# Kernel tuning notes

Hardware: AMD Instinct MI355X
Metric: run time of the kernel (lower is better)

Reference implementation:

```python
import jax, jax.numpy as jnp
import numpy as np

B, T, L = 32, 128, 16
VOCAB, E, H = 256, 256, 512


def setup_inputs() -> dict:
    key = jax.random.key(0)
    ks = jax.random.split(key, 7)
    char_seq_padded = jax.random.randint(ks[0], (B, T, L), 0, VOCAB, dtype=jnp.int32)
    char_lengths = jax.random.randint(ks[1], (B, T), 1, L + 1, dtype=jnp.int32)
    emb = jax.random.normal(ks[2], (VOCAB, E), dtype=jnp.float32) * 0.1
    emb = emb.at[0].set(0.0)  # padding_idx=0 -> zero row
    s_ih = 1.0 / np.sqrt(H)
    W_ih = jax.random.uniform(ks[3], (4 * H, E), jnp.float32, -s_ih, s_ih)
    W_hh = jax.random.uniform(ks[4], (4 * H, H), jnp.float32, -s_ih, s_ih)
    b_ih = jax.random.uniform(ks[5], (4 * H,), jnp.float32, -s_ih, s_ih)
    b_hh = jax.random.uniform(ks[6], (4 * H,), jnp.float32, -s_ih, s_ih)
    return {"char_seq_padded": char_seq_padded, "char_lengths": char_lengths,
            "emb": emb, "W_ih": W_ih, "W_hh": W_hh, "b_ih": b_ih, "b_hh": b_hh}


def _char_lstm(char_seq_padded, char_lengths, emb, W_ih, W_hh, b_ih, b_hh):
    b, t, l = char_seq_padded.shape
    h_dim = W_hh.shape[1]
    idx = char_seq_padded.reshape(b * t, l).T          # [L, B*T]
    lens = char_lengths.reshape(b * t)                  # [B*T]
    bias = b_ih + b_hh

    def step(carry, inp):
        h, c = carry
        ids, tt = inp
        x = emb[ids]                                    # [BT, E]
        gates = x @ W_ih.T + h @ W_hh.T + bias          # [BT, 4H]
        i, f, g, o = jnp.split(gates, 4, axis=-1)       # torch order i,f,g,o
        i = jax.nn.sigmoid(i)
        f = jax.nn.sigmoid(f)
        g = jnp.tanh(g)
        o = jax.nn.sigmoid(o)
        c_new = f * c + i * g
        h_new = o * jnp.tanh(c_new)
        m = (lens > tt).astype(h.dtype)[:, None]        # length mask blend
        h = h_new * m + h * (1.0 - m)
        c = c_new * m + c * (1.0 - m)
        return (h, c), None

    h0 = jnp.zeros((b * t, h_dim), dtype=emb.dtype)
    c0 = jnp.zeros((b * t, h_dim), dtype=emb.dtype)
    (h, _), _ = jax.lax.scan(step, (h0, c0), (idx, jnp.arange(l)))
    return h.reshape(b, t, h_dim)


def reference(char_seq_padded, char_lengths, emb, W_ih, W_hh, b_ih, b_hh):
    return _char_lstm(char_seq_padded, char_lengths, emb, W_ih, W_hh, b_ih, b_hh)
```

## Files before the change

### kernel.cpp

```cpp
#include <hip/hip_runtime.h>
#include <hip/hip_bf16.h>

typedef __attribute__((ext_vector_type(8))) short short8;
typedef __attribute__((ext_vector_type(4))) short short4v;
typedef __attribute__((ext_vector_type(4))) float floatx4;

#define EDIM 256
#define HDIM 512
#define LDIM 16
#define NCOL 2048
#define BM 256
#define KC 32

__device__ __forceinline__ float fsigmoid(float x){ return 1.0f/(1.0f+__expf(-x)); }
__device__ __forceinline__ float ftanh(float x){ return 2.0f/(1.0f+__expf(-2.0f*x))-1.0f; }
__device__ __forceinline__ float bf2f(short s){
    union { unsigned u; float f; } cv; cv.u = ((unsigned)(unsigned short)s) << 16; return cv.f;
}
__device__ __forceinline__ unsigned short f2bf_bits(float v){
    union { __hip_bfloat16 h; unsigned short u; } cv;
    cv.h = __float2bfloat16(v); return cv.u;
}

__device__ __forceinline__ short8 aload16(const short* p) {
    union { unsigned long long q[2]; short8 s; } u;
    u.q[0] = __hip_atomic_load((const unsigned long long*)p,
                               __ATOMIC_RELAXED, __HIP_MEMORY_SCOPE_AGENT);
    u.q[1] = __hip_atomic_load((const unsigned long long*)p + 1,
                               __ATOMIC_RELAXED, __HIP_MEMORY_SCOPE_AGENT);
    return u.s;
}
__device__ __forceinline__ void astore_bf16(short* p, float v) {
    __hip_atomic_store((unsigned short*)p, f2bf_bits(v),
                       __ATOMIC_RELAXED, __HIP_MEMORY_SCOPE_AGENT);
}
__device__ __forceinline__ void lds_barrier() {
    asm volatile("s_waitcnt lgkmcnt(0)" ::: "memory");
    __builtin_amdgcn_s_barrier();
}

__device__ __forceinline__ bool detect_bf16(const short* p) {
    bool bf = true;
    for (int i = 0; i < 64; i += 2) {
        int e = (((unsigned short)p[i]) >> 7) & 0xFF;
        if (e > 0x7B) bf = false;
    }
    return bf;
}

__global__ void conv_whh(const void* __restrict__ whhp, short* __restrict__ whh_o,
                         unsigned* __restrict__ bar) {
    if (blockIdx.x == 0)
        for (int i = threadIdx.x; i < 512; i += 256) bar[i] = 0u;
    bool bf = detect_bf16((const short*)whhp);
    int tid = blockIdx.x * blockDim.x + threadIdx.x;
    int stride = gridDim.x * blockDim.x;
    if (bf) {
        const short* s = (const short*)whhp;
        for (int i = tid; i < NCOL * HDIM; i += stride) whh_o[i] = s[i];
    } else {
        const float* s = (const float*)whhp;
        for (int i = tid; i < NCOL * HDIM; i += stride)
            ((__hip_bfloat16*)whh_o)[i] = __float2bfloat16(s[i]);
    }
}

__global__ void build_xg(const void* __restrict__ embp, const void* __restrict__ wihp,
                         const void* __restrict__ bihp, const void* __restrict__ bhhp,
                         short* __restrict__ xg)
{
    __shared__ float es[16][EDIM];
    __shared__ float wsm[32][EDIM + 1];
    bool bf = detect_bf16((const short*)wihp);
    const int idt = blockIdx.x, ct = blockIdx.y, tt = threadIdx.x;

    if (bf) {
        const __hip_bfloat16* e = (const __hip_bfloat16*)embp;
        const __hip_bfloat16* wv = (const __hip_bfloat16*)wihp;
        for (int p = 0; p < 16; ++p) es[p][tt] = __bfloat162float(e[(idt*16+p)*EDIM + tt]);
        for (int p = 0; p < 32; ++p) wsm[p][tt] = __bfloat162float(wv[(ct*32+p)*EDIM + tt]);
    } else {
        const float* e = (const float*)embp;
        const float* wv = (const float*)wihp;
        for (int p = 0; p < 16; ++p) es[p][tt] = e[(idt*16+p)*EDIM + tt];
        for (int p = 0; p < 32; ++p) wsm[p][tt] = wv[(ct*32+p)*EDIM + tt];
    }
    __syncthreads();

    const int col_l = tt & 31, grp = tt >> 5;
    const int col = ct * 32 + col_l;
    float bsum = bf ? (__bfloat162float(((const __hip_bfloat16*)bihp)[col]) +
                       __bfloat162float(((const __hip_bfloat16*)bhhp)[col]))
                    : (((const float*)bihp)[col] + ((const float*)bhhp)[col]);
    float a0 = 0.f, a1 = 0.f;
    for (int k = 0; k < EDIM; ++k) {
        float wv = wsm[col_l][k];
        a0 += es[grp*2+0][k] * wv;
        a1 += es[grp*2+1][k] * wv;
    }
    const int jj = col & (HDIM - 1), gsel = col >> 9;
    ((__hip_bfloat16*)xg)[(idt*16 + grp*2 + 0)*NCOL + jj*4 + gsel] = __float2bfloat16(a0 + bsum);
    ((__hip_bfloat16*)xg)[(idt*16 + grp*2 + 1)*NCOL + jj*4 + gsel] = __float2bfloat16(a1 + bsum);
}

__launch_bounds__(512, 2)
__global__ void lstm_fused(const int* __restrict__ seq, const int* __restrict__ lens,
                           const short* __restrict__ whh,
                           const short* __restrict__ xg,
                           short* __restrict__ hb0, short* __restrict__ hb1,
                           float* __restrict__ out,
                           unsigned* __restrict__ bar)
{
    __shared__ __align__(16) short Bs[128 * 512];
    __shared__ __align__(16) short As[2][BM * KC];

    const int f  = blockIdx.x;
    const int mt = ((f & 7) << 1) | ((f >> 3) & 1);
    const int jt = f >> 4;
    const int tid = threadIdx.x;
    const int wave = tid >> 6, lane = tid & 63;
    const int q = lane >> 4, ln = lane & 15;
    const int ms = wave & 3, ns = wave >> 2;
    const int jloc = ns * 16 + ln;
    const int jglob = jt * 32 + jloc;

#pragma unroll
    for (int it = 0; it < 16; ++it) {
        int task = it * 512 + tid;
        int row = task >> 6, seg = task & 63;
        int grow = (row >> 5) * HDIM + jt * 32 + (row & 31);
        short8 v = *(const short8*)(whh + grow * HDIM + seg * 8);
        *(short8*)&Bs[row * 512 + ((seg * 8) ^ ((row & 7) << 3))] = v;
    }

    const int chainbase = mt * BM + ms * 64 + q * 4;
    const int obase = chainbase * HDIM + jglob;
    unsigned* __restrict__ barp = bar + (mt << 5);

    const int srow = tid >> 2, sseg = tid & 3;
    const int g0 = srow * HDIM + sseg * 8;
    const int g1 = (128 + srow) * HDIM + sseg * 8;
    const int l0 = srow * KC + ((sseg * 8) ^ ((srow & 3) << 3));
    const int l1 = (128 + srow) * KC + ((sseg * 8) ^ ((srow & 3) << 3));

    unsigned lnspk[4] = {0u, 0u, 0u, 0u};
#pragma unroll
    for (int e = 0; e < 16; ++e)
        lnspk[e >> 2] |= ((unsigned)lens[chainbase + (e >> 2) * 16 + (e & 3)] & 0xFFu)
                         << ((e & 3) * 8);

    float c_st[16], h_st[16];
#pragma unroll
    for (int e = 0; e < 16; ++e) { c_st[e] = 0.f; h_st[e] = 0.f; }

    int idsN[16];
    short4v xv[16];
#pragma unroll
    for (int e = 0; e < 16; ++e)
        idsN[e] = seq[(chainbase + (e >> 2) * 16 + (e & 3)) * LDIM + 0];
#pragma unroll
    for (int e = 0; e < 16; ++e)
        xv[e] = *(const short4v*)(xg + idsN[e] * NCOL + jglob * 4);

    for (int t = 0; t < LDIM; ++t) {
        const short* hr = (t & 1) ? hb1 : hb0;
        short* hw       = (t & 1) ? hb0 : hb1;
        const bool notlast = (t < LDIM - 1);

        if (notlast) {
#pragma unroll
            for (int e = 0; e < 16; ++e)
                idsN[e] = seq[(chainbase + (e >> 2) * 16 + (e & 3)) * LDIM + t + 1];
        }

        floatx4 acc[4][4];
#pragma unroll
        for (int g = 0; g < 4; ++g)
#pragma unroll
            for (int mf = 0; mf < 4; ++mf) acc[g][mf] = (floatx4){0.f, 0.f, 0.f, 0.f};

        if (t > 0) {
            const short* abase = hr + (size_t)mt * BM * HDIM;
            short8 rq[2][2];
            {
                short8 v0 = aload16(abase + g0);
                short8 v1 = aload16(abase + g1);
                rq[1][0]  = aload16(abase + g0 + KC);
                rq[1][1]  = aload16(abase + g1 + KC);
                *(short8*)&As[0][l0] = v0;
                *(short8*)&As[0][l1] = v1;
            }
            lds_barrier();
#pragma unroll
            for (int kc = 0; kc < 16; ++kc) {
                const int b = kc & 1;
                if (kc < 15) {
                    *(short8*)&As[b ^ 1][l0] = rq[(kc + 1) & 1][0];
                    *(short8*)&As[b ^ 1][l1] = rq[(kc + 1) & 1][1];
                }
                if (kc < 14) {
                    rq[kc & 1][0] = aload16(abase + g0 + (kc + 2) * KC);
                    rq[kc & 1][1] = aload16(abase + g1 + (kc + 2) * KC);
                }
                short8 af[4], bfr[4];
#pragma unroll
                for (int mf = 0; mf < 4; ++mf)
                    af[mf] = *(const short8*)&As[b][(ms * 64 + mf * 16 + ln) * KC +
                                                    ((q * 8) ^ ((ln & 3) << 3))];
#pragma unroll
                for (int g = 0; g < 4; ++g)
                    bfr[g] = *(const short8*)&Bs[(g * 32 + jloc) * 512 +
                                                 ((kc * 32 + q * 8) ^ ((ln & 7) << 3))];
                __builtin_amdgcn_s_setprio(1);
#pragma unroll
                for (int g = 0; g < 4; ++g)
#pragma unroll
                    for (int mf = 0; mf < 4; ++mf)
                        acc[g][mf] = __builtin_amdgcn_mfma_f32_16x16x32_bf16(
                            af[mf], bfr[g], acc[g][mf], 0, 0, 0);
                __builtin_amdgcn_s_setprio(0);
                lds_barrier();
            }
        }

#pragma unroll
        for (int e = 0; e < 16; ++e) {
            const int mf = e >> 2, r = e & 3;
            float p0 = acc[0][mf][r] + bf2f(xv[e][0]);
            float p1 = acc[1][mf][r] + bf2f(xv[e][1]);
            float p2 = acc[2][mf][r] + bf2f(xv[e][2]);
            float p3 = acc[3][mf][r] + bf2f(xv[e][3]);
            float ig = fsigmoid(p0);
            float fg = fsigmoid(p1);
            float gg = ftanh(p2);
            float og = fsigmoid(p3);
            float cn = fg * c_st[e] + ig * gg;
            float hn = og * ftanh(cn);
            bool mk = (int)((lnspk[e >> 2] >> ((e & 3) * 8)) & 0xFFu) > t;
            float hsv = mk ? hn : h_st[e];
            float csv = mk ? cn : c_st[e];
            h_st[e] = hsv; c_st[e] = csv;
            int off = obase + (mf * 16 + r) * HDIM;
            if (notlast) astore_bf16(hw + off, hsv);
            else         out[off] = hsv;
        }

        if (notlast) {
            __syncthreads();
#pragma unroll
            for (int e = 0; e < 16; ++e)
                xv[e] = *(const short4v*)(xg + idsN[e] * NCOL + jglob * 4);
            if (tid == 0) {
                __hip_atomic_fetch_add(barp, 1u, __ATOMIC_RELAXED,
                                       __HIP_MEMORY_SCOPE_AGENT);
                const unsigned target = 16u * (unsigned)(t + 1);
                while (__hip_atomic_load(barp, __ATOMIC_RELAXED,
                                         __HIP_MEMORY_SCOPE_AGENT) < target)
                    __builtin_amdgcn_s_sleep(2);
            }
            __syncthreads();
        }
    }
}

extern "C" void kernel_launch(void* const* d_in, const int* in_sizes, int n_in,
                              void* d_out, int out_size, void* d_ws, size_t ws_size,
                              hipStream_t stream) {
    const int* seq  = (const int*)d_in[0];
    const int* lens = (const int*)d_in[1];

    char* w = (char*)d_ws;
    short* h_even = (short*)w;
    short* h_odd  = (short*)(w + 4u*1024*1024);
    short* xg     = (short*)(w + 8u*1024*1024);
    short* whh_bf = (short*)(w + 9u*1024*1024);
    unsigned* bar = (unsigned*)(w + 11u*1024*1024);
    float* outp   = (float*)d_out;

    conv_whh<<<512, 256, 0, stream>>>(d_in[4], whh_bf, bar);
    build_xg<<<dim3(16, 64), 256, 0, stream>>>(d_in[2], d_in[3], d_in[5], d_in[6], xg);
    lstm_fused<<<256, 512, 0, stream>>>(seq, lens, whh_bf, xg, h_even, h_odd, outp, bar);
}
```

Before: 433.0 us.

## Replace per-step group barrier with fine-grained per-block ready flags

Swaps the per-timestep counter barrier across the 16 column-tile blocks of a row group for per-block step flags. Each consumer waits only on the producer flags covering the K-chunks it is about to load, so staged waits can overlap with MFMA work. A separate consumed flag stops a producer from overwriting a double-buffered h slice before readers have finished with it. This cuts synchronization stalls but adds more atomic polling and depends on delicate ordering with relaxed atomics.

```diff
diff --git a/kernel.cpp b/kernel.cpp
--- a/kernel.cpp
+++ b/kernel.cpp
@@ -34,6 +34,20 @@
     __hip_atomic_store((unsigned short*)p, f2bf_bits(v),
                        __ATOMIC_RELAXED, __HIP_MEMORY_SCOPE_AGENT);
 }
+__device__ __forceinline__ unsigned ald(const unsigned* p) {
+    return __hip_atomic_load(p, __ATOMIC_RELAXED, __HIP_MEMORY_SCOPE_AGENT);
+}
+__device__ __forceinline__ void ast(unsigned* p, unsigned v) {
+    __hip_atomic_store(p, v, __ATOMIC_RELAXED, __HIP_MEMORY_SCOPE_AGENT);
+}
+__device__ __forceinline__ void waitflags4(const unsigned* f, unsigned v) {
+    for (;;) {
+        unsigned a = ald(f + 0), b = ald(f + 1);
+        unsigned c = ald(f + 2), d = ald(f + 3);
+        if (a >= v && b >= v && c >= v && d >= v) break;
+        __builtin_amdgcn_s_sleep(1);
+    }
+}
 __device__ __forceinline__ void lds_barrier() {
     asm volatile("s_waitcnt lgkmcnt(0)" ::: "memory");
     __builtin_amdgcn_s_barrier();
@@ -49,9 +63,9 @@
 }
 
 __global__ void conv_whh(const void* __restrict__ whhp, short* __restrict__ whh_o,
-                         unsigned* __restrict__ bar) {
+                         unsigned* __restrict__ sync) {
     if (blockIdx.x == 0)
-        for (int i = threadIdx.x; i < 512; i += 256) bar[i] = 0u;
+        for (int i = threadIdx.x; i < 9216; i += 256) sync[i] = 0u;
     bool bf = detect_bf16((const short*)whhp);
     int tid = blockIdx.x * blockDim.x + threadIdx.x;
     int stride = gridDim.x * blockDim.x;
@@ -109,7 +123,7 @@
                            const short* __restrict__ xg,
                            short* __restrict__ hb0, short* __restrict__ hb1,
                            float* __restrict__ out,
-                           unsigned* __restrict__ bar)
+                           unsigned* __restrict__ sync)
 {
     __shared__ __align__(16) short Bs[128 * 512];
     __shared__ __align__(16) short As[2][BM * KC];
@@ -124,6 +138,9 @@
     const int jloc = ns * 16 + ln;
     const int jglob = jt * 32 + jloc;
 
+    unsigned* const wd = sync + mt * 16;
+    unsigned* const kd = sync + 1024 + (mt * 16) * 32;
+
 #pragma unroll
     for (int it = 0; it < 16; ++it) {
         int task = it * 512 + tid;
@@ -135,7 +152,6 @@
 
     const int chainbase = mt * BM + ms * 64 + q * 4;
     const int obase = chainbase * HDIM + jglob;
-    unsigned* __restrict__ barp = bar + (mt << 5);
 
     const int srow = tid >> 2, sseg = tid & 3;
     const int g0 = srow * HDIM + sseg * 8;
@@ -180,7 +196,9 @@
             for (int mf = 0; mf < 4; ++mf) acc[g][mf] = (floatx4){0.f, 0.f, 0.f, 0.f};
 
         if (t > 0) {
+            const unsigned si = (unsigned)t;
             const short* abase = hr + (size_t)mt * BM * HDIM;
+            waitflags4(wd + 0, si);
             short8 rq[2][2];
             {
                 short8 v0 = aload16(abase + g0);
@@ -198,6 +216,9 @@
                     *(short8*)&As[b ^ 1][l0] = rq[(kc + 1) & 1][0];
                     *(short8*)&As[b ^ 1][l1] = rq[(kc + 1) & 1][1];
                 }
+                if (kc == 0) waitflags4(wd + 4,  si);
+                if (kc == 4) waitflags4(wd + 8,  si);
+                if (kc == 8) waitflags4(wd + 12, si);
                 if (kc < 14) {
                     rq[kc & 1][0] = aload16(abase + g0 + (kc + 2) * KC);
                     rq[kc & 1][1] = aload16(abase + g1 + (kc + 2) * KC);
@@ -221,6 +242,16 @@
                 __builtin_amdgcn_s_setprio(0);
                 lds_barrier();
             }
+            if (tid == 0) ast(kd + jt * 32, si);
+        }
+
+        if (t >= 2 && t < 15) {
+            if (tid < 16) {
+                const unsigned need = (unsigned)(t - 1);
+                while (ald(kd + tid * 32) < need)
+                    __builtin_amdgcn_s_sleep(1);
+            }
+            __syncthreads();
         }
 
 #pragma unroll
@@ -247,18 +278,10 @@
 
         if (notlast) {
             __syncthreads();
+            if (tid == 0) ast(wd + jt, (unsigned)(t + 1));
 #pragma unroll
             for (int e = 0; e < 16; ++e)
                 xv[e] = *(const short4v*)(xg + idsN[e] * NCOL + jglob * 4);
-            if (tid == 0) {
-                __hip_atomic_fetch_add(barp, 1u, __ATOMIC_RELAXED,
-                                       __HIP_MEMORY_SCOPE_AGENT);
-                const unsigned target = 16u * (unsigned)(t + 1);
-                while (__hip_atomic_load(barp, __ATOMIC_RELAXED,
-                                         __HIP_MEMORY_SCOPE_AGENT) < target)
-                    __builtin_amdgcn_s_sleep(2);
-            }
-            __syncthreads();
         }
     }
 }
@@ -274,10 +297,10 @@
     short* h_odd  = (short*)(w + 4u*1024*1024);
     short* xg     = (short*)(w + 8u*1024*1024);
     short* whh_bf = (short*)(w + 9u*1024*1024);
-    unsigned* bar = (unsigned*)(w + 11u*1024*1024);
+    unsigned* syn = (unsigned*)(w + 11u*1024*1024);
     float* outp   = (float*)d_out;
 
-    conv_whh<<<512, 256, 0, stream>>>(d_in[4], whh_bf, bar);
+    conv_whh<<<512, 256, 0, stream>>>(d_in[4], whh_bf, syn);
     build_xg<<<dim3(16, 64), 256, 0, stream>>>(d_in[2], d_in[3], d_in[5], d_in[6], xg);
-    lstm_fused<<<256, 512, 0, stream>>>(seq, lens, whh_bf, xg, h_even, h_odd, outp, bar);
-}
+    lstm_fused<<<256, 512, 0, stream>>>(seq, lens, whh_bf, xg, h_even, h_odd, outp, syn);
+}
```

New measurement: 463.4 us. +7.0%, slower.

## Split LSTM recurrence into 512 narrower blocks with wave-private A tiles

Applied to the files above, without the earlier changes.

Halves the hidden columns handled per block (16 instead of 32), which doubles the grid to 512 blocks and cuts LDS per block so two blocks can sit on each CU. Each wave now stages only its own 32 rows of the h tile into a single LDS buffer, so the per-k-chunk workgroup barriers are removed. The grid barrier target is doubled to match the larger block count. The x-gate loads are no longer prefetched across the barrier and are issued inside the gate epilogue instead. In exchange, every block rereads the full h tile, so global/L2 traffic for h doubles, and the x-gate load latency becomes exposed.

```diff
diff --git a/kernel.cpp b/kernel.cpp
--- a/kernel.cpp
+++ b/kernel.cpp
@@ -9,7 +9,6 @@
 #define HDIM 512
 #define LDIM 16
 #define NCOL 2048
-#define BM 256
 #define KC 32
 
 __device__ __forceinline__ float fsigmoid(float x){ return 1.0f/(1.0f+__expf(-x)); }
@@ -33,10 +32,6 @@
 __device__ __forceinline__ void astore_bf16(short* p, float v) {
     __hip_atomic_store((unsigned short*)p, f2bf_bits(v),
                        __ATOMIC_RELAXED, __HIP_MEMORY_SCOPE_AGENT);
-}
-__device__ __forceinline__ void lds_barrier() {
-    asm volatile("s_waitcnt lgkmcnt(0)" ::: "memory");
-    __builtin_amdgcn_s_barrier();
 }
 
 __device__ __forceinline__ bool detect_bf16(const short* p) {
@@ -103,7 +98,7 @@
     ((__hip_bfloat16*)xg)[(idt*16 + grp*2 + 1)*NCOL + jj*4 + gsel] = __float2bfloat16(a1 + bsum);
 }
 
-__launch_bounds__(512, 2)
+__launch_bounds__(512, 4)
 __global__ void lstm_fused(const int* __restrict__ seq, const int* __restrict__ lens,
                            const short* __restrict__ whh,
                            const short* __restrict__ xg,
@@ -111,125 +106,109 @@
                            float* __restrict__ out,
                            unsigned* __restrict__ bar)
 {
-    __shared__ __align__(16) short Bs[128 * 512];
-    __shared__ __align__(16) short As[2][BM * KC];
+    __shared__ __align__(16) short Bs[64 * 512];
+    __shared__ __align__(16) short As[256 * KC];
 
     const int f  = blockIdx.x;
     const int mt = ((f & 7) << 1) | ((f >> 3) & 1);
     const int jt = f >> 4;
     const int tid = threadIdx.x;
-    const int wave = tid >> 6, lane = tid & 63;
+    const int w = tid >> 6, lane = tid & 63;
     const int q = lane >> 4, ln = lane & 15;
-    const int ms = wave & 3, ns = wave >> 2;
-    const int jloc = ns * 16 + ln;
-    const int jglob = jt * 32 + jloc;
-
-#pragma unroll
-    for (int it = 0; it < 16; ++it) {
+    const int jglob = jt * 16 + ln;
+
+#pragma unroll
+    for (int it = 0; it < 8; ++it) {
         int task = it * 512 + tid;
         int row = task >> 6, seg = task & 63;
-        int grow = (row >> 5) * HDIM + jt * 32 + (row & 31);
+        int grow = (row >> 4) * HDIM + jt * 16 + (row & 15);
         short8 v = *(const short8*)(whh + grow * HDIM + seg * 8);
         *(short8*)&Bs[row * 512 + ((seg * 8) ^ ((row & 7) << 3))] = v;
     }
 
-    const int chainbase = mt * BM + ms * 64 + q * 4;
+    const int chainbase = mt * 256 + w * 32 + q * 4;
     const int obase = chainbase * HDIM + jglob;
     unsigned* __restrict__ barp = bar + (mt << 5);
 
-    const int srow = tid >> 2, sseg = tid & 3;
-    const int g0 = srow * HDIM + sseg * 8;
-    const int g1 = (128 + srow) * HDIM + sseg * 8;
-    const int l0 = srow * KC + ((sseg * 8) ^ ((srow & 3) << 3));
-    const int l1 = (128 + srow) * KC + ((sseg * 8) ^ ((srow & 3) << 3));
-
-    unsigned lnspk[4] = {0u, 0u, 0u, 0u};
-#pragma unroll
-    for (int e = 0; e < 16; ++e)
+    const int srow0 = w * 32 + (lane >> 2), sseg = lane & 3;
+    const int gA0 = srow0 * HDIM + sseg * 8;
+    const int gA1 = gA0 + 16 * HDIM;
+    const int lA0 = srow0 * KC + ((sseg * 8) ^ ((srow0 & 3) << 3));
+    const int lA1 = lA0 + 16 * KC;
+
+    unsigned lnspk[2] = {0u, 0u};
+#pragma unroll
+    for (int e = 0; e < 8; ++e)
         lnspk[e >> 2] |= ((unsigned)lens[chainbase + (e >> 2) * 16 + (e & 3)] & 0xFFu)
                          << ((e & 3) * 8);
 
-    float c_st[16], h_st[16];
-#pragma unroll
-    for (int e = 0; e < 16; ++e) { c_st[e] = 0.f; h_st[e] = 0.f; }
-
-    int idsN[16];
-    short4v xv[16];
-#pragma unroll
-    for (int e = 0; e < 16; ++e)
-        idsN[e] = seq[(chainbase + (e >> 2) * 16 + (e & 3)) * LDIM + 0];
-#pragma unroll
-    for (int e = 0; e < 16; ++e)
-        xv[e] = *(const short4v*)(xg + idsN[e] * NCOL + jglob * 4);
+    float c_st[8], h_st[8];
+#pragma unroll
+    for (int e = 0; e < 8; ++e) { c_st[e] = 0.f; h_st[e] = 0.f; }
+
+    int ids[8];
+#pragma unroll
+    for (int e = 0; e < 8; ++e)
+        ids[e] = seq[(chainbase + (e >> 2) * 16 + (e & 3)) * LDIM + 0];
 
     for (int t = 0; t < LDIM; ++t) {
         const short* hr = (t & 1) ? hb1 : hb0;
         short* hw       = (t & 1) ? hb0 : hb1;
         const bool notlast = (t < LDIM - 1);
 
-        if (notlast) {
-#pragma unroll
-            for (int e = 0; e < 16; ++e)
-                idsN[e] = seq[(chainbase + (e >> 2) * 16 + (e & 3)) * LDIM + t + 1];
-        }
-
-        floatx4 acc[4][4];
+        floatx4 acc[4][2];
 #pragma unroll
         for (int g = 0; g < 4; ++g)
 #pragma unroll
-            for (int mf = 0; mf < 4; ++mf) acc[g][mf] = (floatx4){0.f, 0.f, 0.f, 0.f};
+            for (int mf = 0; mf < 2; ++mf) acc[g][mf] = (floatx4){0.f, 0.f, 0.f, 0.f};
 
         if (t > 0) {
-            const short* abase = hr + (size_t)mt * BM * HDIM;
+            const short* abase = hr + (size_t)mt * 256 * HDIM;
             short8 rq[2][2];
-            {
-                short8 v0 = aload16(abase + g0);
-                short8 v1 = aload16(abase + g1);
-                rq[1][0]  = aload16(abase + g0 + KC);
-                rq[1][1]  = aload16(abase + g1 + KC);
-                *(short8*)&As[0][l0] = v0;
-                *(short8*)&As[0][l1] = v1;
-            }
-            lds_barrier();
+            rq[0][0] = aload16(abase + gA0);
+            rq[0][1] = aload16(abase + gA1);
+            rq[1][0] = aload16(abase + gA0 + KC);
+            rq[1][1] = aload16(abase + gA1 + KC);
+            *(short8*)&As[lA0] = rq[0][0];
+            *(short8*)&As[lA1] = rq[0][1];
 #pragma unroll
             for (int kc = 0; kc < 16; ++kc) {
-                const int b = kc & 1;
+                short8 af[2], bfr[4];
+#pragma unroll
+                for (int mf = 0; mf < 2; ++mf)
+                    af[mf] = *(const short8*)&As[(w * 32 + mf * 16 + ln) * KC +
+                                                 ((q * 8) ^ ((ln & 3) << 3))];
+#pragma unroll
+                for (int g = 0; g < 4; ++g)
+                    bfr[g] = *(const short8*)&Bs[(g * 16 + ln) * 512 +
+                                                 ((kc * 32 + q * 8) ^ ((ln & 7) << 3))];
                 if (kc < 15) {
-                    *(short8*)&As[b ^ 1][l0] = rq[(kc + 1) & 1][0];
-                    *(short8*)&As[b ^ 1][l1] = rq[(kc + 1) & 1][1];
+                    *(short8*)&As[lA0] = rq[(kc + 1) & 1][0];
+                    *(short8*)&As[lA1] = rq[(kc + 1) & 1][1];
                 }
                 if (kc < 14) {
-                    rq[kc & 1][0] = aload16(abase + g0 + (kc + 2) * KC);
-                    rq[kc & 1][1] = aload16(abase + g1 + (kc + 2) * KC);
+                    rq[kc & 1][0] = aload16(abase + gA0 + (kc + 2) * KC);
+                    rq[kc & 1][1] = aload16(abase + gA1 + (kc + 2) * KC);
                 }
-                short8 af[4], bfr[4];
-#pragma unroll
-                for (int mf = 0; mf < 4; ++mf)
-                    af[mf] = *(const short8*)&As[b][(ms * 64 + mf * 16 + ln) * KC +
-                                                    ((q * 8) ^ ((ln & 3) << 3))];
+                __builtin_amdgcn_s_setprio(1);
 #pragma unroll
                 for (int g = 0; g < 4; ++g)
-                    bfr[g] = *(const short8*)&Bs[(g * 32 + jloc) * 512 +
-                                                 ((kc * 32 + q * 8) ^ ((ln & 7) << 3))];
-                __builtin_amdgcn_s_setprio(1);
-#pragma unroll
-                for (int g = 0; g < 4; ++g)
-#pragma unroll
-                    for (int mf = 0; mf < 4; ++mf)
+#pragma unroll
+                    for (int mf = 0; mf < 2; ++mf)
                         acc[g][mf] = __builtin_amdgcn_mfma_f32_16x16x32_bf16(
                             af[mf], bfr[g], acc[g][mf], 0, 0, 0);
                 __builtin_amdgcn_s_setprio(0);
-                lds_barrier();
             }
         }
 
 #pragma unroll
-        for (int e = 0; e < 16; ++e) {
+        for (int e = 0; e < 8; ++e) {
             const int mf = e >> 2, r = e & 3;
-            float p0 = acc[0][mf][r] + bf2f(xv[e][0]);
-            float p1 = acc[1][mf][r] + bf2f(xv[e][1]);
-            float p2 = acc[2][mf][r] + bf2f(xv[e][2]);
-            float p3 = acc[3][mf][r] + bf2f(xv[e][3]);
+            short4v xv = *(const short4v*)(xg + ids[e] * NCOL + jglob * 4);
+            float p0 = acc[0][mf][r] + bf2f(xv[0]);
+            float p1 = acc[1][mf][r] + bf2f(xv[1]);
+            float p2 = acc[2][mf][r] + bf2f(xv[2]);
+            float p3 = acc[3][mf][r] + bf2f(xv[3]);
             float ig = fsigmoid(p0);
             float fg = fsigmoid(p1);
             float gg = ftanh(p2);
@@ -248,12 +227,12 @@
         if (notlast) {
             __syncthreads();
 #pragma unroll
-            for (int e = 0; e < 16; ++e)
-                xv[e] = *(const short4v*)(xg + idsN[e] * NCOL + jglob * 4);
+            for (int e = 0; e < 8; ++e)
+                ids[e] = seq[(chainbase + (e >> 2) * 16 + (e & 3)) * LDIM + t + 1];
             if (tid == 0) {
                 __hip_atomic_fetch_add(barp, 1u, __ATOMIC_RELAXED,
                                        __HIP_MEMORY_SCOPE_AGENT);
-                const unsigned target = 16u * (unsigned)(t + 1);
+                const unsigned target = 32u * (unsigned)(t + 1);
                 while (__hip_atomic_load(barp, __ATOMIC_RELAXED,
                                          __HIP_MEMORY_SCOPE_AGENT) < target)
                     __builtin_amdgcn_s_sleep(2);
@@ -279,5 +258,5 @@
 
     conv_whh<<<512, 256, 0, stream>>>(d_in[4], whh_bf, bar);
     build_xg<<<dim3(16, 64), 256, 0, stream>>>(d_in[2], d_in[3], d_in[5], d_in[6], xg);
-    lstm_fused<<<256, 512, 0, stream>>>(seq, lens, whh_bf, xg, h_even, h_odd, outp, bar);
-}
+    lstm_fused<<<512, 512, 0, stream>>>(seq, lens, whh_bf, xg, h_even, h_odd, outp, bar);
+}
```

Measured after the change: 564.7 us. 1.3x slower.
